# Kernel tuning notes

Measured on AMD Instinct MI355X. Metric: run time of the kernel, lower is better.

Reference implementation:

```python
import jax, jax.numpy as jnp
import numpy as np
import math

D_MODEL = 1024
H = 16
D_K = D_MODEL // H
B = 2
S = 2048
NEG_INF = -1e9


def setup_inputs() -> dict:
    key = jax.random.key(0)
    ks = jax.random.split(key, 12)
    scale = 1.0 / math.sqrt(D_MODEL)
    inp = {
        "q": jax.random.normal(ks[0], (B, S, D_MODEL), jnp.float32),
        "k": jax.random.normal(ks[1], (B, S, D_MODEL), jnp.float32),
        "v": jax.random.normal(ks[2], (B, S, D_MODEL), jnp.float32),
        # causal mask: 1 = keep, 0 = masked (matches torch masked_fill(mask==0))
        "mask": jnp.tril(jnp.ones((S, S), jnp.int32))[None, None],
        "w_q": jax.random.normal(ks[3], (D_MODEL, D_MODEL), jnp.float32) * scale,
        "b_q": jax.random.normal(ks[4], (D_MODEL,), jnp.float32) * scale,
        "w_k": jax.random.normal(ks[5], (D_MODEL, D_MODEL), jnp.float32) * scale,
        "b_k": jax.random.normal(ks[6], (D_MODEL,), jnp.float32) * scale,
        "w_v": jax.random.normal(ks[7], (D_MODEL, D_MODEL), jnp.float32) * scale,
        "b_v": jax.random.normal(ks[8], (D_MODEL,), jnp.float32) * scale,
        "w_o": jax.random.normal(ks[9], (D_MODEL, D_MODEL), jnp.float32) * scale,
        "b_o": jax.random.normal(ks[10], (D_MODEL,), jnp.float32) * scale,
    }
    return inp


def _split_heads(x):
    # (B, S, d_model) -> (B, H, S, d_k)
    b, s, _ = x.shape
    return x.reshape(b, s, H, D_K).transpose(0, 2, 1, 3)


def reference(q, k, v, mask, w_q, b_q, w_k, b_k, w_v, b_v, w_o, b_o):
    qh = _split_heads(q @ w_q.T + b_q)
    kh = _split_heads(k @ w_k.T + b_k)
    vh = _split_heads(v @ w_v.T + b_v)
    scores = jnp.einsum("bhqd,bhkd->bhqk", qh, kh) / math.sqrt(D_K)
    scores = jnp.where(mask == 0, NEG_INF, scores)
    attn = jax.nn.softmax(scores, axis=-1)
    ctx = jnp.einsum("bhqk,bhkd->bhqd", attn, vh)  # (B,H,S,d_k)
    ctx = ctx.transpose(0, 2, 1, 3).reshape(q.shape[0], -1, D_MODEL)
    out = ctx @ w_o.T + b_o
    return out, attn
```

## Files before the change

### kernel.cpp

```cpp
#include <hip/hip_runtime.h>

#define D_MODEL 1024
#define NHEAD 16
#define DK 64
#define BATCH 2
#define SEQ 2048
constexpr int MROWS = BATCH * SEQ;

typedef __attribute__((ext_vector_type(8))) short short8;
typedef __attribute__((ext_vector_type(4))) float f32x4;

__device__ inline unsigned short f2bf(float f) {
  union { float f; unsigned int u; } c; c.f = f;
  unsigned int u = c.u;
  return (unsigned short)((u + 0x7fffu + ((u >> 16) & 1u)) >> 16);
}

__device__ inline uint4 pack8(float4 a, float4 b) {
  union { unsigned short h[8]; uint4 v; } t;
  t.h[0] = f2bf(a.x); t.h[1] = f2bf(a.y); t.h[2] = f2bf(a.z); t.h[3] = f2bf(a.w);
  t.h[4] = f2bf(b.x); t.h[5] = f2bf(b.y); t.h[6] = f2bf(b.z); t.h[7] = f2bf(b.w);
  return t.v;
}

template <int EPI, typename AT>
__global__ __launch_bounds__(256) void gemm_mfma(
    const AT* __restrict__ A, const float* __restrict__ W,
    const float* __restrict__ bias, void* __restrict__ outp,
    int M, int N, int K) {
  __shared__ unsigned short Asb[128 * 32];
  __shared__ unsigned short Bsb[128 * 32];

  const int tid = threadIdx.x;
  const int lane = tid & 63;
  const int wv = tid >> 6;
  const int q15 = lane & 15, g = lane >> 4;
  const int wr = wv >> 1, wc = wv & 1;
  const int m0 = blockIdx.y * 128, n0 = blockIdx.x * 128;

  f32x4 acc[4][4] = {};

  for (int k0 = 0; k0 < K; k0 += 32) {
    __syncthreads();
#pragma unroll
    for (int uu = 0; uu < 2; ++uu) {
      int u = tid + uu * 256;
      int row = u >> 2, c = u & 3;
      int cs = c ^ (row & 3) ^ ((row >> 2) & 3);
      if constexpr (sizeof(AT) == 4) {
        const float* s = (const float*)A + (size_t)(m0 + row) * K + k0 + c * 8;
        float4 f0 = *(const float4*)s, f1 = *(const float4*)(s + 4);
        *(uint4*)&Asb[row * 32 + cs * 8] = pack8(f0, f1);
      } else {
        *(uint4*)&Asb[row * 32 + cs * 8] =
            *(const uint4*)((const unsigned short*)A + (size_t)(m0 + row) * K + k0 + c * 8);
      }
      const float* sw = W + (size_t)(n0 + row) * K + k0 + c * 8;
      float4 w0 = *(const float4*)sw, w1 = *(const float4*)(sw + 4);
      *(uint4*)&Bsb[row * 32 + cs * 8] = pack8(w0, w1);
    }
    __syncthreads();

    short8 af[4], bfr[4];
#pragma unroll
    for (int rb = 0; rb < 4; ++rb) {
      int row = wr * 64 + rb * 16 + q15;
      int cs = g ^ (row & 3) ^ ((row >> 2) & 3);
      af[rb] = *(const short8*)&Asb[row * 32 + cs * 8];
    }
#pragma unroll
    for (int cb = 0; cb < 4; ++cb) {
      int row = wc * 64 + cb * 16 + q15;
      int cs = g ^ (row & 3) ^ ((row >> 2) & 3);
      bfr[cb] = *(const short8*)&Bsb[row * 32 + cs * 8];
    }
#pragma unroll
    for (int rb = 0; rb < 4; ++rb)
#pragma unroll
      for (int cb = 0; cb < 4; ++cb)
        acc[rb][cb] = __builtin_amdgcn_mfma_f32_16x16x32_bf16(
            af[rb], bfr[cb], acc[rb][cb], 0, 0, 0);
  }

#pragma unroll
  for (int cb = 0; cb < 4; ++cb) {
    int n = n0 + wc * 64 + cb * 16 + q15;
    float bn = bias[n];
#pragma unroll
    for (int rb = 0; rb < 4; ++rb) {
#pragma unroll
      for (int reg = 0; reg < 4; ++reg) {
        int m = m0 + wr * 64 + rb * 16 + g * 4 + reg;
        float v = acc[rb][cb][reg] + bn;
        if constexpr (EPI == 0) {
          ((float*)outp)[(size_t)m * N + n] = v;
        } else if constexpr (EPI == 1) {
          int b = m >> 11, s = m & (SEQ - 1);
          int h = n >> 6, d = n & 63;
          ((unsigned short*)outp)[(((size_t)(b * NHEAD + h) * SEQ) + s) * DK + d] = f2bf(v);
        } else {
          int b = m >> 11, s = m & (SEQ - 1);
          int h = n >> 6, d = n & 63;
          ((unsigned short*)outp)[(((size_t)(b * NHEAD + h) * DK) + d) * SEQ + s] = f2bf(v);
        }
      }
    }
  }
}

__global__ __launch_bounds__(256) void attn_mfma(
    const unsigned short* __restrict__ qh, const unsigned short* __restrict__ kh,
    const unsigned short* __restrict__ vt, float* __restrict__ attn,
    unsigned short* __restrict__ ctx) {
  __shared__ unsigned short Pl[64 * 72];

  const int tid = threadIdx.x;
  const int lane = tid & 63;
  const int w = tid >> 6;
  const int q15 = lane & 15, g = lane >> 4;
  const int qt = (gridDim.x - 1) - blockIdx.x;
  const int bh = blockIdx.y;
  const float scale = 0.125f;

  const size_t khead = (size_t)bh * SEQ * DK;
  const int qrow0 = qt * 64 + w * 16;

  const unsigned short* qp = qh + khead + (size_t)(qrow0 + q15) * DK + g * 8;
  short8 aq0 = *(const short8*)qp;
  short8 aq1 = *(const short8*)(qp + 32);

  float m[4], l[4];
#pragma unroll
  for (int r = 0; r < 4; ++r) { m[r] = -1e30f; l[r] = 0.f; }

  for (int kt = 0; kt <= qt; ++kt) {
    const unsigned short* kb = kh + khead + (size_t)(kt * 64) * DK;
    f32x4 sv[4];
#pragma unroll
    for (int jb = 0; jb < 4; ++jb) {
      const unsigned short* kp = kb + (size_t)(jb * 16 + q15) * DK + g * 8;
      short8 b0 = *(const short8*)kp;
      short8 b1 = *(const short8*)(kp + 32);
      f32x4 z = {};
      z = __builtin_amdgcn_mfma_f32_16x16x32_bf16(aq0, b0, z, 0, 0, 0);
      sv[jb] = __builtin_amdgcn_mfma_f32_16x16x32_bf16(aq1, b1, z, 0, 0, 0);
    }
    const bool diag = (kt == qt);
#pragma unroll
    for (int r = 0; r < 4; ++r) {
      int rowg = qrow0 + g * 4 + r;
      float t[4];
      float tmax = -1e30f;
#pragma unroll
      for (int jb = 0; jb < 4; ++jb) {
        int col = kt * 64 + jb * 16 + q15;
        bool valid = !diag || (col <= rowg);
        t[jb] = valid ? sv[jb][r] * scale : -1e30f;
        tmax = fmaxf(tmax, t[jb]);
      }
      float mn = fmaxf(m[r], tmax);
      float corr = __expf(m[r] - mn);
      float add = 0.f;
#pragma unroll
      for (int jb = 0; jb < 4; ++jb) {
        int col = kt * 64 + jb * 16 + q15;
        bool valid = !diag || (col <= rowg);
        add += valid ? __expf(t[jb] - mn) : 0.f;
      }
      l[r] = l[r] * corr + add;
      m[r] = mn;
    }
  }

#pragma unroll
  for (int off = 1; off < 16; off <<= 1) {
#pragma unroll
    for (int r = 0; r < 4; ++r) {
      float mo = __shfl_xor(m[r], off);
      float lo = __shfl_xor(l[r], off);
      float mn = fmaxf(m[r], mo);
      l[r] = l[r] * __expf(m[r] - mn) + lo * __expf(mo - mn);
      m[r] = mn;
    }
  }
  float inv[4];
#pragma unroll
  for (int r = 0; r < 4; ++r) inv[r] = 1.0f / l[r];

  f32x4 cacc[4] = {};
  const size_t abase = ((size_t)bh * SEQ + qt * 64 + w * 16) * SEQ;
  const unsigned short* vhead = vt + (size_t)bh * DK * SEQ;

  for (int kt = 0; kt <= qt; ++kt) {
    const unsigned short* kb = kh + khead + (size_t)(kt * 64) * DK;
    f32x4 sv[4];
#pragma unroll
    for (int jb = 0; jb < 4; ++jb) {
      const unsigned short* kp = kb + (size_t)(jb * 16 + q15) * DK + g * 8;
      short8 b0 = *(const short8*)kp;
      short8 b1 = *(const short8*)(kp + 32);
      f32x4 z = {};
      z = __builtin_amdgcn_mfma_f32_16x16x32_bf16(aq0, b0, z, 0, 0, 0);
      sv[jb] = __builtin_amdgcn_mfma_f32_16x16x32_bf16(aq1, b1, z, 0, 0, 0);
    }
    const bool diag = (kt == qt);
#pragma unroll
    for (int jb = 0; jb < 4; ++jb) {
      int col = kt * 64 + jb * 16 + q15;
#pragma unroll
      for (int r = 0; r < 4; ++r) {
        int rowg = qrow0 + g * 4 + r;
        bool valid = !diag || (col <= rowg);
        float p = valid ? __expf(sv[jb][r] * scale - m[r]) * inv[r] : 0.f;
        attn[abase + (size_t)(g * 4 + r) * SEQ + col] = p;
        Pl[(w * 16 + g * 4 + r) * 72 + jb * 16 + q15] = f2bf(p);
      }
    }
#pragma unroll
    for (int ks = 0; ks < 2; ++ks) {
      short8 pa = *(const short8*)&Pl[(w * 16 + q15) * 72 + ks * 32 + g * 8];
#pragma unroll
      for (int jd = 0; jd < 4; ++jd) {
        const unsigned short* vp =
            vhead + (size_t)(jd * 16 + q15) * SEQ + kt * 64 + ks * 32 + g * 8;
        short8 vb = *(const short8*)vp;
        cacc[jd] = __builtin_amdgcn_mfma_f32_16x16x32_bf16(pa, vb, cacc[jd], 0, 0, 0);
      }
    }
  }

  {
    int trow = tid & 63, seg = tid >> 6;
    const size_t zbase = ((size_t)bh * SEQ + qt * 64 + trow) * SEQ;
    float4 zz = make_float4(0.f, 0.f, 0.f, 0.f);
    for (int kt = qt + 1; kt < SEQ / 64; ++kt) {
      float* p = attn + zbase + kt * 64 + seg * 16;
      *(float4*)(p + 0) = zz; *(float4*)(p + 4) = zz;
      *(float4*)(p + 8) = zz; *(float4*)(p + 12) = zz;
    }
  }

  const int b = bh >> 4, h = bh & (NHEAD - 1);
#pragma unroll
  for (int jd = 0; jd < 4; ++jd) {
#pragma unroll
    for (int reg = 0; reg < 4; ++reg) {
      int s = qt * 64 + w * 16 + g * 4 + reg;
      int d = jd * 16 + q15;
      ctx[((size_t)b * SEQ + s) * D_MODEL + h * DK + d] = f2bf(cacc[jd][reg]);
    }
  }
}

extern "C" void kernel_launch(void* const* d_in, const int* in_sizes, int n_in,
                              void* d_out, int out_size, void* d_ws,
                              size_t ws_size, hipStream_t stream) {
  const float* q = (const float*)d_in[0];
  const float* k = (const float*)d_in[1];
  const float* v = (const float*)d_in[2];
  const float* w_q = (const float*)d_in[4];
  const float* b_q = (const float*)d_in[5];
  const float* w_k = (const float*)d_in[6];
  const float* b_k = (const float*)d_in[7];
  const float* w_v = (const float*)d_in[8];
  const float* b_v = (const float*)d_in[9];
  const float* w_o = (const float*)d_in[10];
  const float* b_o = (const float*)d_in[11];

  float* out = (float*)d_out;
  float* attn = out + (size_t)BATCH * SEQ * D_MODEL;

  const size_t te = (size_t)BATCH * SEQ * D_MODEL;
  unsigned short* qh = (unsigned short*)d_ws;
  unsigned short* kh = qh + te;
  unsigned short* vt = kh + te;
  unsigned short* ctx = vt + te;

  dim3 gproj(D_MODEL / 128, MROWS / 128);
  gemm_mfma<1, float><<<gproj, 256, 0, stream>>>(q, w_q, b_q, qh, MROWS, D_MODEL, D_MODEL);
  gemm_mfma<1, float><<<gproj, 256, 0, stream>>>(k, w_k, b_k, kh, MROWS, D_MODEL, D_MODEL);
  gemm_mfma<2, float><<<gproj, 256, 0, stream>>>(v, w_v, b_v, vt, MROWS, D_MODEL, D_MODEL);

  attn_mfma<<<dim3(SEQ / 64, BATCH * NHEAD), 256, 0, stream>>>(qh, kh, vt, attn, ctx);

  gemm_mfma<0, unsigned short><<<gproj, 256, 0, stream>>>(ctx, w_o, b_o, out,
                                                          MROWS, D_MODEL, D_MODEL);
}
```

Measured before the change: 1.220 ms.

## Pre-convert inputs to bf16, use direct-to-LDS GEMM loads, restructure attention kernel

Adds conversion kernels that cast activations and weights to bf16 once, so the projection GEMMs can load tiles straight into LDS with global_load_lds instead of converting during each load. The attention kernel swaps the MFMA operand order so each lane owns one query row. That lets probabilities and context be written as contiguous vector stores, and K fragments are prefetched one tile ahead. It also drops running-max tracking and computes the softmax denominator with a plain exponential sum, removing the max/rescale work. This risks overflow for large scores. Blocks are remapped so each XCD handles its own heads. The unswizzled LDS layout may add bank conflicts, and the conversion kernels add extra launches and memory traffic.

```diff
diff --git a/kernel.cpp b/kernel.cpp
--- a/kernel.cpp
+++ b/kernel.cpp
@@ -23,11 +23,32 @@
   return t.v;
 }
 
-template <int EPI, typename AT>
-__global__ __launch_bounds__(256) void gemm_mfma(
-    const AT* __restrict__ A, const float* __restrict__ W,
-    const float* __restrict__ bias, void* __restrict__ outp,
-    int M, int N, int K) {
+__device__ inline uint2 pack4(f32x4 p) {
+  union { unsigned short h[4]; uint2 v; } t;
+  t.h[0] = f2bf(p[0]); t.h[1] = f2bf(p[1]); t.h[2] = f2bf(p[2]); t.h[3] = f2bf(p[3]);
+  return t.v;
+}
+
+__device__ inline void gload_lds16(const void* g, void* l) {
+  __builtin_amdgcn_global_load_lds((const __attribute__((address_space(1))) void*)g,
+                                   (__attribute__((address_space(3))) void*)l, 16, 0, 0);
+}
+
+__global__ __launch_bounds__(256) void cvt_bf16(const float* __restrict__ src,
+                                                unsigned short* __restrict__ dst,
+                                                int n8) {
+  int i = blockIdx.x * 256 + threadIdx.x;
+  if (i < n8) {
+    const float4* s = (const float4*)(src + (size_t)i * 8);
+    float4 a = s[0], b = s[1];
+    *(uint4*)(dst + (size_t)i * 8) = pack8(a, b);
+  }
+}
+
+template <int EPI>
+__global__ __launch_bounds__(256) void gemm_bf16(
+    const unsigned short* __restrict__ A, const unsigned short* __restrict__ W,
+    const float* __restrict__ bias, void* __restrict__ outp, int M, int N, int K) {
   __shared__ unsigned short Asb[128 * 32];
   __shared__ unsigned short Bsb[128 * 32];
 
@@ -43,43 +64,29 @@
   for (int k0 = 0; k0 < K; k0 += 32) {
     __syncthreads();
 #pragma unroll
-    for (int uu = 0; uu < 2; ++uu) {
-      int u = tid + uu * 256;
-      int row = u >> 2, c = u & 3;
-      int cs = c ^ (row & 3) ^ ((row >> 2) & 3);
-      if constexpr (sizeof(AT) == 4) {
-        const float* s = (const float*)A + (size_t)(m0 + row) * K + k0 + c * 8;
-        float4 f0 = *(const float4*)s, f1 = *(const float4*)(s + 4);
-        *(uint4*)&Asb[row * 32 + cs * 8] = pack8(f0, f1);
-      } else {
-        *(uint4*)&Asb[row * 32 + cs * 8] =
-            *(const uint4*)((const unsigned short*)A + (size_t)(m0 + row) * K + k0 + c * 8);
-      }
-      const float* sw = W + (size_t)(n0 + row) * K + k0 + c * 8;
-      float4 w0 = *(const float4*)sw, w1 = *(const float4*)(sw + 4);
-      *(uint4*)&Bsb[row * 32 + cs * 8] = pack8(w0, w1);
+    for (int c = 0; c < 2; ++c) {
+      int off = (wv * 2 + c) * 1024 + lane * 16;
+      int row = off >> 6, inb = off & 63;
+      const char* ga = (const char*)A + (size_t)(m0 + row) * (K * 2) + k0 * 2 + inb;
+      gload_lds16(ga, (char*)Asb + (wv * 2 + c) * 1024);
+      const char* gb = (const char*)W + (size_t)(n0 + row) * (K * 2) + k0 * 2 + inb;
+      gload_lds16(gb, (char*)Bsb + (wv * 2 + c) * 1024);
     }
     __syncthreads();
 
-    short8 af[4], bfr[4];
-#pragma unroll
-    for (int rb = 0; rb < 4; ++rb) {
-      int row = wr * 64 + rb * 16 + q15;
-      int cs = g ^ (row & 3) ^ ((row >> 2) & 3);
-      af[rb] = *(const short8*)&Asb[row * 32 + cs * 8];
-    }
-#pragma unroll
-    for (int cb = 0; cb < 4; ++cb) {
-      int row = wc * 64 + cb * 16 + q15;
-      int cs = g ^ (row & 3) ^ ((row >> 2) & 3);
-      bfr[cb] = *(const short8*)&Bsb[row * 32 + cs * 8];
-    }
+    short8 af[4], bfv[4];
+#pragma unroll
+    for (int rb = 0; rb < 4; ++rb)
+      af[rb] = *(const short8*)&Asb[(wr * 64 + rb * 16 + q15) * 32 + g * 8];
+#pragma unroll
+    for (int cb = 0; cb < 4; ++cb)
+      bfv[cb] = *(const short8*)&Bsb[(wc * 64 + cb * 16 + q15) * 32 + g * 8];
 #pragma unroll
     for (int rb = 0; rb < 4; ++rb)
 #pragma unroll
       for (int cb = 0; cb < 4; ++cb)
         acc[rb][cb] = __builtin_amdgcn_mfma_f32_16x16x32_bf16(
-            af[rb], bfr[cb], acc[rb][cb], 0, 0, 0);
+            af[rb], bfv[cb], acc[rb][cb], 0, 0, 0);
   }
 
 #pragma unroll
@@ -95,12 +102,10 @@
         if constexpr (EPI == 0) {
           ((float*)outp)[(size_t)m * N + n] = v;
         } else if constexpr (EPI == 1) {
-          int b = m >> 11, s = m & (SEQ - 1);
-          int h = n >> 6, d = n & 63;
+          int b = m >> 11, s = m & (SEQ - 1), h = n >> 6, d = n & 63;
           ((unsigned short*)outp)[(((size_t)(b * NHEAD + h) * SEQ) + s) * DK + d] = f2bf(v);
         } else {
-          int b = m >> 11, s = m & (SEQ - 1);
-          int h = n >> 6, d = n & 63;
+          int b = m >> 11, s = m & (SEQ - 1), h = n >> 6, d = n & 63;
           ((unsigned short*)outp)[(((size_t)(b * NHEAD + h) * DK) + d) * SEQ + s] = f2bf(v);
         }
       }
@@ -112,120 +117,122 @@
     const unsigned short* __restrict__ qh, const unsigned short* __restrict__ kh,
     const unsigned short* __restrict__ vt, float* __restrict__ attn,
     unsigned short* __restrict__ ctx) {
-  __shared__ unsigned short Pl[64 * 72];
+  __shared__ unsigned short Pl[4][16][72];
 
   const int tid = threadIdx.x;
   const int lane = tid & 63;
   const int w = tid >> 6;
   const int q15 = lane & 15, g = lane >> 4;
-  const int qt = (gridDim.x - 1) - blockIdx.x;
-  const int bh = blockIdx.y;
+  const int id = blockIdx.x;
+  const int xcd = id & 7, slot = id >> 3;
+  const int bh = xcd + 8 * (slot >> 5);
+  const int qt = 31 - (slot & 31);
   const float scale = 0.125f;
 
   const size_t khead = (size_t)bh * SEQ * DK;
-  const int qrow0 = qt * 64 + w * 16;
-
-  const unsigned short* qp = qh + khead + (size_t)(qrow0 + q15) * DK + g * 8;
-  short8 aq0 = *(const short8*)qp;
-  short8 aq1 = *(const short8*)(qp + 32);
-
-  float m[4], l[4];
-#pragma unroll
-  for (int r = 0; r < 4; ++r) { m[r] = -1e30f; l[r] = 0.f; }
-
+  const int qg = qt * 64 + w * 16 + q15;
+
+  const unsigned short* qp = qh + khead + (size_t)qg * DK + g * 8;
+  short8 bq0 = *(const short8*)qp;
+  short8 bq1 = *(const short8*)(qp + 32);
+
+  const unsigned short* kbase = kh + khead;
+
+  float l = 0.f;
+  short8 kf[8];
+#pragma unroll
+  for (int jb = 0; jb < 4; ++jb) {
+    const unsigned short* kp = kbase + (size_t)(jb * 16 + q15) * DK + g * 8;
+    kf[jb * 2] = *(const short8*)kp;
+    kf[jb * 2 + 1] = *(const short8*)(kp + 32);
+  }
   for (int kt = 0; kt <= qt; ++kt) {
-    const unsigned short* kb = kh + khead + (size_t)(kt * 64) * DK;
+    short8 kn[8];
+    if (kt < qt) {
+      const unsigned short* kb = kbase + (size_t)((kt + 1) * 64) * DK;
+#pragma unroll
+      for (int jb = 0; jb < 4; ++jb) {
+        const unsigned short* kp = kb + (size_t)(jb * 16 + q15) * DK + g * 8;
+        kn[jb * 2] = *(const short8*)kp;
+        kn[jb * 2 + 1] = *(const short8*)(kp + 32);
+      }
+    }
     f32x4 sv[4];
 #pragma unroll
     for (int jb = 0; jb < 4; ++jb) {
-      const unsigned short* kp = kb + (size_t)(jb * 16 + q15) * DK + g * 8;
-      short8 b0 = *(const short8*)kp;
-      short8 b1 = *(const short8*)(kp + 32);
       f32x4 z = {};
-      z = __builtin_amdgcn_mfma_f32_16x16x32_bf16(aq0, b0, z, 0, 0, 0);
-      sv[jb] = __builtin_amdgcn_mfma_f32_16x16x32_bf16(aq1, b1, z, 0, 0, 0);
-    }
-    const bool diag = (kt == qt);
-#pragma unroll
-    for (int r = 0; r < 4; ++r) {
-      int rowg = qrow0 + g * 4 + r;
-      float t[4];
-      float tmax = -1e30f;
+      z = __builtin_amdgcn_mfma_f32_16x16x32_bf16(kf[jb * 2], bq0, z, 0, 0, 0);
+      sv[jb] = __builtin_amdgcn_mfma_f32_16x16x32_bf16(kf[jb * 2 + 1], bq1, z, 0, 0, 0);
+    }
+#pragma unroll
+    for (int jb = 0; jb < 4; ++jb)
+#pragma unroll
+      for (int r = 0; r < 4; ++r) {
+        int kidx = kt * 64 + jb * 16 + g * 4 + r;
+        l += (kidx <= qg) ? __expf(sv[jb][r] * scale) : 0.f;
+      }
+    if (kt < qt) {
+#pragma unroll
+      for (int u = 0; u < 8; ++u) kf[u] = kn[u];
+    }
+  }
+  l += __shfl_xor(l, 16);
+  l += __shfl_xor(l, 32);
+  const float inv = 1.0f / l;
+
+  f32x4 cacc[4] = {};
+  const unsigned short* vhead = vt + (size_t)bh * DK * SEQ;
+  float* arow = attn + ((size_t)bh * SEQ + qg) * SEQ;
+
+#pragma unroll
+  for (int jb = 0; jb < 4; ++jb) {
+    const unsigned short* kp = kbase + (size_t)(jb * 16 + q15) * DK + g * 8;
+    kf[jb * 2] = *(const short8*)kp;
+    kf[jb * 2 + 1] = *(const short8*)(kp + 32);
+  }
+  for (int kt = 0; kt <= qt; ++kt) {
+    short8 kn[8];
+    if (kt < qt) {
+      const unsigned short* kb = kbase + (size_t)((kt + 1) * 64) * DK;
 #pragma unroll
       for (int jb = 0; jb < 4; ++jb) {
-        int col = kt * 64 + jb * 16 + q15;
-        bool valid = !diag || (col <= rowg);
-        t[jb] = valid ? sv[jb][r] * scale : -1e30f;
-        tmax = fmaxf(tmax, t[jb]);
-      }
-      float mn = fmaxf(m[r], tmax);
-      float corr = __expf(m[r] - mn);
-      float add = 0.f;
-#pragma unroll
-      for (int jb = 0; jb < 4; ++jb) {
-        int col = kt * 64 + jb * 16 + q15;
-        bool valid = !diag || (col <= rowg);
-        add += valid ? __expf(t[jb] - mn) : 0.f;
-      }
-      l[r] = l[r] * corr + add;
-      m[r] = mn;
-    }
-  }
-
-#pragma unroll
-  for (int off = 1; off < 16; off <<= 1) {
-#pragma unroll
-    for (int r = 0; r < 4; ++r) {
-      float mo = __shfl_xor(m[r], off);
-      float lo = __shfl_xor(l[r], off);
-      float mn = fmaxf(m[r], mo);
-      l[r] = l[r] * __expf(m[r] - mn) + lo * __expf(mo - mn);
-      m[r] = mn;
-    }
-  }
-  float inv[4];
-#pragma unroll
-  for (int r = 0; r < 4; ++r) inv[r] = 1.0f / l[r];
-
-  f32x4 cacc[4] = {};
-  const size_t abase = ((size_t)bh * SEQ + qt * 64 + w * 16) * SEQ;
-  const unsigned short* vhead = vt + (size_t)bh * DK * SEQ;
-
-  for (int kt = 0; kt <= qt; ++kt) {
-    const unsigned short* kb = kh + khead + (size_t)(kt * 64) * DK;
+        const unsigned short* kp = kb + (size_t)(jb * 16 + q15) * DK + g * 8;
+        kn[jb * 2] = *(const short8*)kp;
+        kn[jb * 2 + 1] = *(const short8*)(kp + 32);
+      }
+    }
     f32x4 sv[4];
 #pragma unroll
     for (int jb = 0; jb < 4; ++jb) {
-      const unsigned short* kp = kb + (size_t)(jb * 16 + q15) * DK + g * 8;
-      short8 b0 = *(const short8*)kp;
-      short8 b1 = *(const short8*)(kp + 32);
       f32x4 z = {};
-      z = __builtin_amdgcn_mfma_f32_16x16x32_bf16(aq0, b0, z, 0, 0, 0);
-      sv[jb] = __builtin_amdgcn_mfma_f32_16x16x32_bf16(aq1, b1, z, 0, 0, 0);
-    }
-    const bool diag = (kt == qt);
+      z = __builtin_amdgcn_mfma_f32_16x16x32_bf16(kf[jb * 2], bq0, z, 0, 0, 0);
+      sv[jb] = __builtin_amdgcn_mfma_f32_16x16x32_bf16(kf[jb * 2 + 1], bq1, z, 0, 0, 0);
+    }
 #pragma unroll
     for (int jb = 0; jb < 4; ++jb) {
-      int col = kt * 64 + jb * 16 + q15;
+      f32x4 p;
 #pragma unroll
       for (int r = 0; r < 4; ++r) {
-        int rowg = qrow0 + g * 4 + r;
-        bool valid = !diag || (col <= rowg);
-        float p = valid ? __expf(sv[jb][r] * scale - m[r]) * inv[r] : 0.f;
-        attn[abase + (size_t)(g * 4 + r) * SEQ + col] = p;
-        Pl[(w * 16 + g * 4 + r) * 72 + jb * 16 + q15] = f2bf(p);
-      }
+        int kidx = kt * 64 + jb * 16 + g * 4 + r;
+        p[r] = (kidx <= qg) ? __expf(sv[jb][r] * scale) * inv : 0.f;
+      }
+      *(f32x4*)&arow[kt * 64 + jb * 16 + g * 4] = p;
+      *(uint2*)&Pl[w][q15][jb * 16 + g * 4] = pack4(p);
     }
 #pragma unroll
     for (int ks = 0; ks < 2; ++ks) {
-      short8 pa = *(const short8*)&Pl[(w * 16 + q15) * 72 + ks * 32 + g * 8];
+      short8 pb = *(const short8*)&Pl[w][q15][ks * 32 + g * 8];
 #pragma unroll
       for (int jd = 0; jd < 4; ++jd) {
         const unsigned short* vp =
             vhead + (size_t)(jd * 16 + q15) * SEQ + kt * 64 + ks * 32 + g * 8;
         short8 vb = *(const short8*)vp;
-        cacc[jd] = __builtin_amdgcn_mfma_f32_16x16x32_bf16(pa, vb, cacc[jd], 0, 0, 0);
-      }
+        cacc[jd] = __builtin_amdgcn_mfma_f32_16x16x32_bf16(vb, pb, cacc[jd], 0, 0, 0);
+      }
+    }
+    if (kt < qt) {
+#pragma unroll
+      for (int u = 0; u < 8; ++u) kf[u] = kn[u];
     }
   }
 
@@ -233,23 +240,18 @@
     int trow = tid & 63, seg = tid >> 6;
     const size_t zbase = ((size_t)bh * SEQ + qt * 64 + trow) * SEQ;
     float4 zz = make_float4(0.f, 0.f, 0.f, 0.f);
-    for (int kt = qt + 1; kt < SEQ / 64; ++kt) {
-      float* p = attn + zbase + kt * 64 + seg * 16;
+    for (int kt2 = qt + 1; kt2 < SEQ / 64; ++kt2) {
+      float* p = attn + zbase + kt2 * 64 + seg * 16;
       *(float4*)(p + 0) = zz; *(float4*)(p + 4) = zz;
       *(float4*)(p + 8) = zz; *(float4*)(p + 12) = zz;
     }
   }
 
   const int b = bh >> 4, h = bh & (NHEAD - 1);
-#pragma unroll
-  for (int jd = 0; jd < 4; ++jd) {
-#pragma unroll
-    for (int reg = 0; reg < 4; ++reg) {
-      int s = qt * 64 + w * 16 + g * 4 + reg;
-      int d = jd * 16 + q15;
-      ctx[((size_t)b * SEQ + s) * D_MODEL + h * DK + d] = f2bf(cacc[jd][reg]);
-    }
-  }
+  unsigned short* crow = ctx + ((size_t)b * SEQ + qg) * D_MODEL + h * DK;
+#pragma unroll
+  for (int jd = 0; jd < 4; ++jd)
+    *(uint2*)&crow[jd * 16 + g * 4] = pack4(cacc[jd]);
 }
 
 extern "C" void kernel_launch(void* const* d_in, const int* in_sizes, int n_in,
@@ -271,18 +273,33 @@
   float* attn = out + (size_t)BATCH * SEQ * D_MODEL;
 
   const size_t te = (size_t)BATCH * SEQ * D_MODEL;
-  unsigned short* qh = (unsigned short*)d_ws;
-  unsigned short* kh = qh + te;
-  unsigned short* vt = kh + te;
-  unsigned short* ctx = vt + te;
+  const size_t dm2 = (size_t)D_MODEL * D_MODEL;
+  unsigned short* qb = (unsigned short*)d_ws;
+  unsigned short* kb = qb + te;
+  unsigned short* vb = kb + te;
+  unsigned short* wqb = vb + te;
+  unsigned short* wkb = wqb + dm2;
+  unsigned short* wvb = wkb + dm2;
+  unsigned short* wob = wvb + dm2;
+  unsigned short* qhb = wob + dm2;
+  unsigned short* khb = qhb + te;
+  unsigned short* vtb = khb + te;
+  unsigned short* ctxb = qb;
+
+  cvt_bf16<<<(int)(te / 8 / 256), 256, 0, stream>>>(q, qb, (int)(te / 8));
+  cvt_bf16<<<(int)(te / 8 / 256), 256, 0, stream>>>(k, kb, (int)(te / 8));
+  cvt_bf16<<<(int)(te / 8 / 256), 256, 0, stream>>>(v, vb, (int)(te / 8));
+  cvt_bf16<<<(int)(dm2 / 8 / 256), 256, 0, stream>>>(w_q, wqb, (int)(dm2 / 8));
+  cvt_bf16<<<(int)(dm2 / 8 / 256), 256, 0, stream>>>(w_k, wkb, (int)(dm2 / 8));
+  cvt_bf16<<<(int)(dm2 / 8 / 256), 256, 0, stream>>>(w_v, wvb, (int)(dm2 / 8));
+  cvt_bf16<<<(int)(dm2 / 8 / 256), 256, 0, stream>>>(w_o, wob, (int)(dm2 / 8));
 
   dim3 gproj(D_MODEL / 128, MROWS / 128);
-  gemm_mfma<1, float><<<gproj, 256, 0, stream>>>(q, w_q, b_q, qh, MROWS, D_MODEL, D_MODEL);
-  gemm_mfma<1, float><<<gproj, 256, 0, stream>>>(k, w_k, b_k, kh, MROWS, D_MODEL, D_MODEL);
-  gemm_mfma<2, float><<<gproj, 256, 0, stream>>>(v, w_v, b_v, vt, MROWS, D_MODEL, D_MODEL);
-
-  attn_mfma<<<dim3(SEQ / 64, BATCH * NHEAD), 256, 0, stream>>>(qh, kh, vt, attn, ctx);
-
-  gemm_mfma<0, unsigned short><<<gproj, 256, 0, stream>>>(ctx, w_o, b_o, out,
-                                                          MROWS, D_MODEL, D_MODEL);
-}
+  gemm_bf16<1><<<gproj, 256, 0, stream>>>(qb, wqb, b_q, qhb, MROWS, D_MODEL, D_MODEL);
+  gemm_bf16<1><<<gproj, 256, 0, stream>>>(kb, wkb, b_k, khb, MROWS, D_MODEL, D_MODEL);
+  gemm_bf16<2><<<gproj, 256, 0, stream>>>(vb, wvb, b_v, vtb, MROWS, D_MODEL, D_MODEL);
+
+  attn_mfma<<<1024, 256, 0, stream>>>(qhb, khb, vtb, attn, ctxb);
+
+  gemm_bf16<0><<<gproj, 256, 0, stream>>>(ctxb, wob, b_o, out, MROWS, D_MODEL, D_MODEL);
+}
```

Result: faster. 1.133 ms (-7.1%).
